# Kernel optimization log

Measured on AMD Instinct MI355X. Metric: run time of the kernel, lower is better.

Reference implementation:

```python
import jax, jax.numpy as jnp
import numpy as np

N, E, G = 100000, 400000, 4096
H, C = 4, 32            # heads, hidden_dim per head
D_OUT = H * C           # 128
NODE_D, EDGE_D = 38, 13
DEC_H, OUT_D = 64, 1
NEG_SLOPE = 0.2
LN_EPS = 1e-5


def setup_inputs() -> dict:
    key = jax.random.key(0)
    ks = jax.random.split(key, 40)
    r = lambda k, s: jax.random.normal(k, s, jnp.float32) * 0.1
    inp = {
        "x": jax.random.normal(ks[0], (N, NODE_D), jnp.float32),
        "edge_index": jax.random.randint(ks[1], (2, E), 0, N),
        "edge_attr": jax.random.uniform(ks[2], (E, EDGE_D), jnp.float32),
        "batch": jnp.sort(jax.random.randint(ks[3], (N,), 0, G)),
        # --- block 1 (in=38) ---
        "Wl1": r(ks[4], (NODE_D, D_OUT)), "bl1": jnp.zeros((D_OUT,), jnp.float32),
        "Wr1": r(ks[5], (NODE_D, D_OUT)), "br1": jnp.zeros((D_OUT,), jnp.float32),
        "We1": r(ks[6], (EDGE_D, D_OUT)),
        "att1": r(ks[7], (H, C)), "ab1": jnp.zeros((D_OUT,), jnp.float32),
        "ln_g1": jnp.ones((D_OUT,), jnp.float32), "ln_b1": jnp.zeros((D_OUT,), jnp.float32),
        "Wres": r(ks[8], (NODE_D, D_OUT)), "bres": jnp.zeros((D_OUT,), jnp.float32),
        # --- block 2 (in=128, residual = identity) ---
        "Wl2": r(ks[9], (D_OUT, D_OUT)), "bl2": jnp.zeros((D_OUT,), jnp.float32),
        "Wr2": r(ks[10], (D_OUT, D_OUT)), "br2": jnp.zeros((D_OUT,), jnp.float32),
        "We2": r(ks[11], (EDGE_D, D_OUT)),
        "att2": r(ks[12], (H, C)), "ab2": jnp.zeros((D_OUT,), jnp.float32),
        "ln_g2": jnp.ones((D_OUT,), jnp.float32), "ln_b2": jnp.zeros((D_OUT,), jnp.float32),
        # --- readout MLP ---
        "Wd1": r(ks[13], (D_OUT, DEC_H)), "bd1": jnp.zeros((DEC_H,), jnp.float32),
        "Wd2": r(ks[14], (DEC_H, OUT_D)), "bd2": jnp.zeros((OUT_D,), jnp.float32),
    }
    return inp


def _segment_softmax(logits, seg, n):
    m = jax.ops.segment_max(logits, seg, num_segments=n)
    ex = jnp.exp(logits - m[seg])
    s = jax.ops.segment_sum(ex, seg, num_segments=n)
    return ex / s[seg]


def _gatv2(x, src, dst, e_feat, Wl, bl, Wr, br, We, att, ab):
    n = x.shape[0]
    xl = (x @ Wl + bl).reshape(n, H, C)   # source transform
    xr = (x @ Wr + br).reshape(n, H, C)   # target transform
    ee = (e_feat @ We).reshape(-1, H, C)  # edge transform
    z = jax.nn.leaky_relu(xl[src] + xr[dst] + ee, NEG_SLOPE)  # [E,H,C]
    logits = jnp.einsum('ehc,hc->eh', z, att)                 # [E,H]
    alpha = _segment_softmax(logits, dst, n)                  # softmax over target nbhd
    out = jax.ops.segment_sum(xl[src] * alpha[..., None], dst, num_segments=n)
    return out.reshape(n, D_OUT) + ab


def _layernorm(h, g, b):
    mu = jnp.mean(h, -1, keepdims=True)
    d = h - mu
    v = jnp.mean(d * d, -1, keepdims=True)
    return d * jax.lax.rsqrt(v + LN_EPS) * g + b


def reference(x, edge_index, edge_attr, batch,
              Wl1, bl1, Wr1, br1, We1, att1, ab1, ln_g1, ln_b1, Wres, bres,
              Wl2, bl2, Wr2, br2, We2, att2, ab2, ln_g2, ln_b2,
              Wd1, bd1, Wd2, bd2):
    src, dst = edge_index[0], edge_index[1]
    n = x.shape[0]
    # add_self_loops(fill_value='mean'): self-loop edge attr = mean of incoming edge attrs
    deg = jax.ops.segment_sum(jnp.ones((src.shape[0],), x.dtype), dst, num_segments=n)
    loop_attr = jax.ops.segment_sum(edge_attr, dst, num_segments=n) / jnp.clip(deg, 1.0)[:, None]
    nodes = jnp.arange(n)
    src_a = jnp.concatenate([src, nodes])
    dst_a = jnp.concatenate([dst, nodes])
    ea = jnp.concatenate([edge_attr, loop_attr], axis=0)

    # block 1
    h = _gatv2(x, src_a, dst_a, ea, Wl1, bl1, Wr1, br1, We1, att1, ab1)
    h = jax.nn.elu(h)
    h = _layernorm(h + (x @ Wres + bres), ln_g1, ln_b1)
    # block 2 (identity residual)
    h2 = _gatv2(h, src_a, dst_a, ea, Wl2, bl2, Wr2, br2, We2, att2, ab2)
    h2 = jax.nn.elu(h2)
    h2 = _layernorm(h2 + h, ln_g2, ln_b2)

    # global mean pool over graphs
    cnt = jax.ops.segment_sum(jnp.ones((n,), x.dtype), batch, num_segments=G)
    g = jax.ops.segment_sum(h2, batch, num_segments=G) / jnp.clip(cnt, 1.0)[:, None]

    return jax.nn.relu(g @ Wd1 + bd1) @ Wd2 + bd2
```

## Files before the change

kernel.cpp:

```cpp
#include <hip/hip_runtime.h>

typedef unsigned short u16;
typedef unsigned int   u32;
typedef __attribute__((ext_vector_type(8))) short short8;
typedef __attribute__((ext_vector_type(4))) float float4v;
typedef __attribute__((ext_vector_type(2))) float float2v;

#define NODE_D   38
#define EDGE_D   13
#define D_OUT    128
#define NEG_SLOPE 0.2f
#define LN_EPS   1e-5f

__device__ __forceinline__ float bf2f(u16 v) { return __uint_as_float(((u32)v) << 16); }
__device__ __forceinline__ u16 f2bf(float f) {
    u32 u = __float_as_uint(f);
    u += 0x7fffu + ((u >> 16) & 1u);
    return (u16)(u >> 16);
}

template <int CTRL>
__device__ __forceinline__ float dpp_radd(float x) {
    int t = __builtin_amdgcn_update_dpp(0, __float_as_int(x), CTRL, 0xf, 0xf, true);
    return x + __int_as_float(t);
}
__device__ __forceinline__ float reduce16(float p) {
    p = dpp_radd<0xB1>(p);
    p = dpp_radd<0x4E>(p);
    p = dpp_radd<0x124>(p);
    p = dpp_radd<0x128>(p);
    return p;
}
__device__ __forceinline__ float reduce64(float v) {
    v = reduce16(v);
    v += __shfl_xor(v, 16, 64);
    v += __shfl_xor(v, 32, 64);
    return v;
}

__global__ void k_pre(const int* __restrict__ dst, int E, int* __restrict__ deg,
                      const int* __restrict__ batch, int N, int G, int* __restrict__ goff,
                      const float* __restrict__ x, u16* __restrict__ xb) {
    int i = blockIdx.x * blockDim.x + threadIdx.x;
    if (i < E) atomicAdd(deg + dst[i], 1);
    if (i < N) {
        int b = batch[i];
        int prev = (i == 0) ? -1 : batch[i - 1];
        for (int g = prev + 1; g <= b; g++) goff[g] = i;
        if (i == N - 1)
            for (int g = b + 1; g <= G; g++) goff[g] = N;
    }
    if (i < N * 32) {
        int n = i >> 5, kk = (i & 31) * 2;
        float f0 = (kk < NODE_D) ? x[(size_t)n * NODE_D + kk] : 0.f;
        float f1 = (kk + 1 < NODE_D) ? x[(size_t)n * NODE_D + kk + 1] : 0.f;
        ((u32*)xb)[(size_t)n * 32 + (i & 31)] = (u32)f2bf(f0) | ((u32)f2bf(f1) << 16);
    }
}

#define SCAN_CHUNK 1024
__global__ void k_scan1(const int* __restrict__ cnt, int N, int addone, int* __restrict__ bsum) {
    __shared__ int sh[256];
    int base = blockIdx.x * SCAN_CHUNK;
    int t = threadIdx.x;
    int s = 0;
#pragma unroll
    for (int i = 0; i < 4; i++) { int idx = base + t * 4 + i; if (idx < N) s += cnt[idx] + addone; }
    sh[t] = s; __syncthreads();
    for (int ofs = 128; ofs > 0; ofs >>= 1) {
        if (t < ofs) sh[t] += sh[t + ofs];
        __syncthreads();
    }
    if (t == 0) bsum[blockIdx.x] = sh[0];
}
__global__ void k_scan2(const int* __restrict__ bsum, int nb, int* __restrict__ boff) {
    __shared__ int sh[256];
    int t = threadIdx.x;
    if (nb <= 256) {
        int v = (t < nb) ? bsum[t] : 0;
        sh[t] = v; __syncthreads();
        for (int ofs = 1; ofs < 256; ofs <<= 1) {
            int x = (t >= ofs) ? sh[t - ofs] : 0;
            __syncthreads();
            sh[t] += x;
            __syncthreads();
        }
        if (t < nb) boff[t] = sh[t] - v;
        if (t == nb - 1) boff[nb] = sh[t];
    } else if (t == 0) {
        int run = 0;
        for (int i = 0; i < nb; i++) { boff[i] = run; run += bsum[i]; }
        boff[nb] = run;
    }
}
__global__ void k_scan3(const int* __restrict__ cnt, int N, int addone,
                        const int* __restrict__ boff, int nb, int* __restrict__ off) {
    __shared__ int wtot[4];
    int base = blockIdx.x * SCAN_CHUNK;
    int t = threadIdx.x;
    int lane = t & 63, w = t >> 6;
    int v[4]; int s = 0;
#pragma unroll
    for (int i = 0; i < 4; i++) { int idx = base + t * 4 + i; v[i] = (idx < N) ? cnt[idx] + addone : 0; s += v[i]; }
    int inc = s;
#pragma unroll
    for (int ofs = 1; ofs < 64; ofs <<= 1) {
        int x = __shfl_up(inc, ofs, 64);
        if (lane >= ofs) inc += x;
    }
    if (lane == 63) wtot[w] = inc;
    __syncthreads();
    int wofs = 0;
    for (int i = 0; i < w; i++) wofs += wtot[i];
    int run = boff[blockIdx.x] + wofs + (inc - s);
#pragma unroll
    for (int i = 0; i < 4; i++) {
        int idx = base + t * 4 + i;
        if (idx < N) off[idx] = run;
        run += v[i];
    }
    if (blockIdx.x == 0 && t == 0) off[N] = boff[nb];
}

__global__ void k_fill(const int* __restrict__ src, const int* __restrict__ dst,
                       const float* __restrict__ eattr, int E,
                       const int* __restrict__ csr_off, int* __restrict__ fill,
                       int* __restrict__ csr_src, u16* __restrict__ A) {
    int e = blockIdx.x * blockDim.x + threadIdx.x;
    if (e >= E) return;
    int d = dst[e];
    int pos = csr_off[d] + atomicAdd(fill + d, 1);
    csr_src[pos] = src[e];
    u16 row[16];
#pragma unroll
    for (int k = 0; k < EDGE_D; k++) row[k] = f2bf(eattr[(size_t)e * EDGE_D + k]);
#pragma unroll
    for (int k = EDGE_D; k < 16; k++) row[k] = 0;
    uint4* rp = (uint4*)(A + (size_t)pos * 16);
    rp[0] = (uint4){(u32)row[0] | ((u32)row[1] << 16), (u32)row[2] | ((u32)row[3] << 16),
                    (u32)row[4] | ((u32)row[5] << 16), (u32)row[6] | ((u32)row[7] << 16)};
    rp[1] = (uint4){(u32)row[8] | ((u32)row[9] << 16), (u32)row[10] | ((u32)row[11] << 16),
                    (u32)row[12] | ((u32)row[13] << 16), (u32)row[14] | ((u32)row[15] << 16)};
}

__global__ void k_self(const int* __restrict__ csr_off, int N,
                       int* __restrict__ csr_src, u16* __restrict__ A) {
    int tid = blockIdx.x * blockDim.x + threadIdx.x;
    if (tid >= N * 16) return;
    int n = tid >> 4, k = tid & 15;
    int b = csr_off[n], e2 = csr_off[n + 1] - 1;
    u16 v = 0;
    if (k < EDGE_D) {
        float s = 0.f;
        for (int j = b; j < e2; j++) s += bf2f(A[(size_t)j * 16 + k]);
        v = f2bf(s / fmaxf((float)(e2 - b), 1.f));
    }
    A[(size_t)e2 * 16 + k] = v;
    if (k == 0) csr_src[e2] = n;
}

template <int KPAD, int CT, int KREAL, bool IN_BF16>
__global__ __launch_bounds__(256) void k_tf_mfma(
    const void* __restrict__ in_v,
    const float* __restrict__ W0, const float* __restrict__ b0,
    const float* __restrict__ W1, const float* __restrict__ b1,
    const float* __restrict__ W2, const float* __restrict__ b2,
    u16* __restrict__ o0, u16* __restrict__ o1, u16* __restrict__ o2,
    int N) {
    constexpr int RS = KPAD + 8;
    __shared__ u16 Bsw[CT * 16 * RS];
    __shared__ float bsh[CT * 16];
    const float* Ws[3] = {W0, W1, W2};
    const float* bs[3] = {b0, b1, b2};
    u16* outs[3] = {o0, o1, o2};
    int t = threadIdx.x;
    for (int i = t; i < CT * 16 * KPAD; i += 256) {
        int c = i / KPAD, k = i - c * KPAD;
        float v = (k < KREAL) ? Ws[c >> 7][(size_t)k * 128 + (c & 127)] : 0.f;
        Bsw[c * RS + k] = f2bf(v);
    }
    for (int i = t; i < CT * 16; i += 256) bsh[i] = bs[i >> 7][i & 127];
    __syncthreads();

    int wid = t >> 6, lane = t & 63;
    int quad = lane >> 4, m = lane & 15;

    for (int g0 = blockIdx.x * 64; g0 < N; g0 += gridDim.x * 64) {
        int na = g0 + wid * 16 + m;
        if (na > N - 1) na = N - 1;
        short8 a[KPAD / 32];
        if (IN_BF16) {
            const u16* in = (const u16*)in_v;
#pragma unroll
            for (int kc = 0; kc < KPAD / 32; kc++)
                a[kc] = *(const short8*)(in + (size_t)na * KPAD + kc * 32 + quad * 8);
        } else {
            const float* in = (const float*)in_v;
#pragma unroll
            for (int kc = 0; kc < KPAD / 32; kc++)
#pragma unroll
                for (int j = 0; j < 8; j++) {
                    int k = kc * 32 + quad * 8 + j;
                    float v = (k < KREAL) ? in[(size_t)na * KREAL + k] : 0.f;
                    a[kc][j] = (short)f2bf(v);
                }
        }
        float4v acc[CT];
#pragma unroll
        for (int ct = 0; ct < CT; ct++) acc[ct] = (float4v){0.f, 0.f, 0.f, 0.f};
#pragma unroll
        for (int ct = 0; ct < CT; ct++) {
#pragma unroll
            for (int kc = 0; kc < KPAD / 32; kc++) {
                short8 b = *(const short8*)(&Bsw[(ct * 16 + m) * RS + kc * 32 + quad * 8]);
                acc[ct] = __builtin_amdgcn_mfma_f32_16x16x32_bf16(a[kc], b, acc[ct], 0, 0, 0);
            }
        }
#pragma unroll
        for (int ct = 0; ct < CT; ct++) {
            int col = ct * 16 + m;
            u16* op = outs[col >> 7];
            int cc = col & 127;
            float bv = bsh[col];
#pragma unroll
            for (int r = 0; r < 4; r++) {
                int node = g0 + wid * 16 + quad * 4 + r;
                if (node < N) op[(size_t)node * 128 + cc] = f2bf(acc[ct][r] + bv);
            }
        }
    }
}

__global__ __launch_bounds__(256) void k_gat(
    const int* __restrict__ csr_off, const int* __restrict__ csr_src,
    const u16* __restrict__ A_csr,
    const u16* __restrict__ xl, const u16* __restrict__ xr,
    const u16* __restrict__ res, const float* __restrict__ We,
    const float* __restrict__ att, const float* __restrict__ ab,
    const float* __restrict__ lng, const float* __restrict__ lnb,
    u16* __restrict__ hout, int N, int npw) {
    int t = threadIdx.x;
    int wid = t >> 6, lane = t & 63;
    int wave = blockIdx.x * 4 + wid;
    int n0 = wave * npw;
    if (n0 >= N) return;
    int n1 = n0 + npw; if (n1 > N) n1 = N;

    float2v we2[EDGE_D];
#pragma unroll
    for (int k = 0; k < EDGE_D; k++)
        we2[k] = (float2v){We[k * D_OUT + 2 * lane], We[k * D_OUT + 2 * lane + 1]};
    float a0 = att[2 * lane], a1 = att[2 * lane + 1];
    float abv0 = ab[2 * lane], abv1 = ab[2 * lane + 1];
    float lg0 = lng[2 * lane], lg1 = lng[2 * lane + 1];
    float lb0 = lnb[2 * lane], lb1 = lnb[2 * lane + 1];

    const u32* xl32 = (const u32*)xl;
    const u32* xr32 = (const u32*)xr;
    int wbeg = csr_off[n0];
    int wend = csr_off[n1];
    int nedge = wend - wbeg;

    auto finish = [&](int n, float ssum, float2v acc2) {
        float inv = 1.f / ssum;
        float o0 = acc2[0] * inv + abv0;
        float o1 = acc2[1] * inv + abv1;
        o0 = (o0 > 0.f) ? o0 : (__expf(o0) - 1.f);
        o1 = (o1 > 0.f) ? o1 : (__expf(o1) - 1.f);
        u32 rw = ((const u32*)res)[(size_t)n * 64 + lane];
        o0 += bf2f((u16)(rw & 0xffff));
        o1 += bf2f((u16)(rw >> 16));
        float sm = reduce64(o0 + o1);
        float mu = sm * (1.f / 128.f);
        float d0 = o0 - mu, d1 = o1 - mu;
        float vv = reduce64(d0 * d0 + d1 * d1);
        float rs = rsqrtf(vv * (1.f / 128.f) + LN_EPS);
        float h0 = d0 * rs * lg0 + lb0;
        float h1 = d1 * rs * lg1 + lb1;
        ((u32*)hout)[(size_t)n * 64 + lane] = (u32)f2bf(h0) | ((u32)f2bf(h1) << 16);
    };

    const float2v z0v = (float2v){0.f, 0.f};

    if (nedge <= 64) {
        int last = nedge - 1;
        int sv = csr_src[wbeg + ((lane < nedge) ? lane : last)];
        int f0 = __builtin_amdgcn_readlane(sv, 0);
        int f1 = __builtin_amdgcn_readlane(sv, (1 <= last) ? 1 : last);
        int f2 = __builtin_amdgcn_readlane(sv, (2 <= last) ? 2 : last);
        int f3 = __builtin_amdgcn_readlane(sv, (3 <= last) ? 3 : last);
        u32 xw0 = xl32[(size_t)f0 * 64 + lane];
        u32 xw1 = xl32[(size_t)f1 * 64 + lane];
        u32 xw2 = xl32[(size_t)f2 * 64 + lane];
        u32 xw3 = xl32[(size_t)f3 * 64 + lane];
        const uint4* ap = (const uint4*)(A_csr + (size_t)wbeg * 16);
        uint4 aq0 = ap[0], aq1 = ap[1];

        int i = wbeg;
        for (int n = n0; n < n1; n++) {
            int end = csr_off[n + 1];
            u32 xrw = xr32[(size_t)n * 64 + lane];
            float2v xr2 = (float2v){bf2f((u16)(xrw & 0xffff)), bf2f((u16)(xrw >> 16))};
            float ssum = 0.f;
            float2v acc2 = (float2v){0.f, 0.f};
            for (; i < end; i++) {
                int j4 = i + 4 - wbeg; if (j4 > last) j4 = last;
                int f4 = __builtin_amdgcn_readlane(sv, j4);
                u32 xwN = xl32[(size_t)f4 * 64 + lane];
                int j1n = i + 1 - wbeg; if (j1n > last) j1n = last;
                const uint4* apn = (const uint4*)(A_csr + (size_t)(wbeg + j1n) * 16);
                uint4 an0 = apn[0], an1 = apn[1];

                u32 dw[8] = {aq0.x, aq0.y, aq0.z, aq0.w, aq1.x, aq1.y, aq1.z, aq1.w};
                float2v eeA = (float2v){0.f, 0.f}, eeB = (float2v){0.f, 0.f};
#pragma unroll
                for (int k = 0; k < EDGE_D; k++) {
                    u32 d = dw[k >> 1];
                    float av = __uint_as_float((k & 1) ? (d & 0xffff0000u) : (d << 16));
                    if ((k >> 1) & 1) eeB += we2[k] * av;
                    else             eeA += we2[k] * av;
                }
                float2v xs = (float2v){bf2f((u16)(xw0 & 0xffff)), bf2f((u16)(xw0 >> 16))};
                float2v z = (xs + xr2) + (eeA + eeB);
                float2v lz = __builtin_elementwise_max(z, z0v) + __builtin_elementwise_min(z, z0v) * NEG_SLOPE;
                float p = lz[0] * a0 + lz[1] * a1;
                p = reduce16(p);
                float wgt = __expf(p);
                ssum += wgt;
                acc2 += xs * wgt;
                xw0 = xw1; xw1 = xw2; xw2 = xw3; xw3 = xwN;
                aq0 = an0; aq1 = an1;
            }
            finish(n, ssum, acc2);
        }
    } else {
        int cl = wend - 1;
        int f = csr_src[wbeg];
        u32 xw = xl32[(size_t)f * 64 + lane];
        const uint4* ap = (const uint4*)(A_csr + (size_t)wbeg * 16);
        uint4 aq0 = ap[0], aq1 = ap[1];
        int i = wbeg;
        for (int n = n0; n < n1; n++) {
            int end = csr_off[n + 1];
            u32 xrw = xr32[(size_t)n * 64 + lane];
            float2v xr2 = (float2v){bf2f((u16)(xrw & 0xffff)), bf2f((u16)(xrw >> 16))};
            float ssum = 0.f;
            float2v acc2 = (float2v){0.f, 0.f};
            for (; i < end; i++) {
                u32 xwc = xw; uint4 q0 = aq0, q1 = aq1;
                int ip = (i + 1 < wend) ? i + 1 : cl;
                f = csr_src[ip];
                xw = xl32[(size_t)f * 64 + lane];
                const uint4* ap2 = (const uint4*)(A_csr + (size_t)ip * 16);
                aq0 = ap2[0]; aq1 = ap2[1];
                u32 dw[8] = {q0.x, q0.y, q0.z, q0.w, q1.x, q1.y, q1.z, q1.w};
                float2v eeA = (float2v){0.f, 0.f}, eeB = (float2v){0.f, 0.f};
#pragma unroll
                for (int k = 0; k < EDGE_D; k++) {
                    u32 d = dw[k >> 1];
                    float av = __uint_as_float((k & 1) ? (d & 0xffff0000u) : (d << 16));
                    if ((k >> 1) & 1) eeB += we2[k] * av;
                    else             eeA += we2[k] * av;
                }
                float2v xs = (float2v){bf2f((u16)(xwc & 0xffff)), bf2f((u16)(xwc >> 16))};
                float2v z = (xs + xr2) + (eeA + eeB);
                float2v lz = __builtin_elementwise_max(z, z0v) + __builtin_elementwise_min(z, z0v) * NEG_SLOPE;
                float p = lz[0] * a0 + lz[1] * a1;
                p = reduce16(p);
                float wgt = __expf(p);
                ssum += wgt;
                acc2 += xs * wgt;
            }
            finish(n, ssum, acc2);
        }
    }
}

__global__ __launch_bounds__(256) void k_pool_read(
    const u16* __restrict__ h2, const int* __restrict__ goff,
    const float* __restrict__ Wd1, const float* __restrict__ bd1,
    const float* __restrict__ Wd2, const float* __restrict__ bd2,
    float* __restrict__ out, int G) {
    __shared__ float acc4[4][128];
    __shared__ float psh[128];
    __shared__ float rsh[2][64];
    int g = blockIdx.x;
    int t = threadIdx.x;
    int lane = t & 63, sw = t >> 6;
    int b = goff[g], e = goff[g + 1];
    const u32* h32 = (const u32*)h2;
    float s0 = 0.f, s1 = 0.f;
    for (int n = b + sw; n < e; n += 4) {
        u32 w = h32[(size_t)n * 64 + lane];
        s0 += bf2f((u16)(w & 0xffff));
        s1 += bf2f((u16)(w >> 16));
    }
    acc4[sw][2 * lane] = s0;
    acc4[sw][2 * lane + 1] = s1;
    __syncthreads();
    if (t < 128) {
        float v = acc4[0][t] + acc4[1][t] + acc4[2][t] + acc4[3][t];
        psh[t] = v / fmaxf((float)(e - b), 1.f);
    }
    __syncthreads();
    if (t < 128) {
        int j = t & 63, hw = t >> 6;
        float acc = (hw == 0) ? bd1[j] : 0.f;
        int k0 = hw * 64;
        for (int k = k0; k < k0 + 64; k++)
            acc += psh[k] * Wd1[k * 64 + j];
        rsh[hw][j] = acc;
    }
    __syncthreads();
    if (t < 64) {
        float a = fmaxf(rsh[0][t] + rsh[1][t], 0.f);
        float v = a * Wd2[t];
#pragma unroll
        for (int mk = 1; mk < 64; mk <<= 1) v += __shfl_xor(v, mk, 64);
        if (t == 0) out[g] = v + bd2[0];
    }
}

extern "C" void kernel_launch(void* const* d_in, const int* in_sizes, int n_in,
                              void* d_out, int out_size, void* d_ws, size_t ws_size,
                              hipStream_t stream) {
    const float* x     = (const float*)d_in[0];
    const int*   eidx  = (const int*)d_in[1];
    const float* eattr = (const float*)d_in[2];
    const int*   batch = (const int*)d_in[3];
    const float* Wl1 = (const float*)d_in[4],  *bl1 = (const float*)d_in[5];
    const float* Wr1 = (const float*)d_in[6],  *br1 = (const float*)d_in[7];
    const float* We1 = (const float*)d_in[8],  *att1 = (const float*)d_in[9],  *ab1 = (const float*)d_in[10];
    const float* lng1 = (const float*)d_in[11], *lnb1 = (const float*)d_in[12];
    const float* Wres = (const float*)d_in[13], *bres = (const float*)d_in[14];
    const float* Wl2 = (const float*)d_in[15], *bl2 = (const float*)d_in[16];
    const float* Wr2 = (const float*)d_in[17], *br2 = (const float*)d_in[18];
    const float* We2 = (const float*)d_in[19], *att2 = (const float*)d_in[20], *ab2 = (const float*)d_in[21];
    const float* lng2 = (const float*)d_in[22], *lnb2 = (const float*)d_in[23];
    const float* Wd1 = (const float*)d_in[24], *bd1 = (const float*)d_in[25];
    const float* Wd2 = (const float*)d_in[26], *bd2 = (const float*)d_in[27];

    int N = in_sizes[0] / NODE_D;
    int E = in_sizes[1] / 2;
    int G = out_size;
    int EN = E + N;
    const int* src = eidx;
    const int* dst = eidx + E;

    char* w = (char*)d_ws;
    auto alloc = [&](size_t bytes) -> char* {
        char* p = w;
        w += (bytes + 255) & ~(size_t)255;
        return p;
    };
    int NB = (N + SCAN_CHUNK - 1) / SCAN_CHUNK;
    int*   csr_off  = (int*)alloc((size_t)(N + 1) * 4);
    int*   csr_src  = (int*)alloc((size_t)EN * 4);
    u16*   A_csr    = (u16*)alloc((size_t)(EN + 64) * 16 * 2);
    u16*   xb       = (u16*)alloc((size_t)N * 64 * 2);
    u16*   xlb      = (u16*)alloc((size_t)N * D_OUT * 2);
    u16*   xrb      = (u16*)alloc((size_t)N * D_OUT * 2);
    u16*   resb     = (u16*)alloc((size_t)N * D_OUT * 2);
    u16*   hb       = (u16*)alloc((size_t)N * D_OUT * 2);
    int*   goff     = (int*)alloc((size_t)(G + 1) * 4);
    size_t szN = ((size_t)N * 4 + 255) & ~(size_t)255;
    char*  zp   = alloc(2 * szN);
    int*   deg  = (int*)zp;
    int*   fill = (int*)(zp + szN);
    int*   bsum = (int*)alloc((size_t)(NB + 1) * 4);
    int*   boff = (int*)alloc((size_t)(NB + 1) * 4);

    hipMemsetAsync(zp, 0, 2 * szN, stream);

    int mx = (E > N * 32) ? E : N * 32;
    k_pre<<<(mx + 255) / 256, 256, 0, stream>>>(dst, E, deg, batch, N, G, goff, x, xb);

    k_scan1<<<NB, 256, 0, stream>>>(deg, N, 1, bsum);
    k_scan2<<<1, 256, 0, stream>>>(bsum, NB, boff);
    k_scan3<<<NB, 256, 0, stream>>>(deg, N, 1, boff, NB, csr_off);
    k_fill<<<(E + 255) / 256, 256, 0, stream>>>(src, dst, eattr, E, csr_off, fill, csr_src, A_csr);
    k_self<<<((size_t)N * 16 + 255) / 256, 256, 0, stream>>>(csr_off, N, csr_src, A_csr);

    int npw = 4;
    int gblocks = (N + npw * 4 - 1) / (npw * 4);

    k_tf_mfma<64, 24, NODE_D, true><<<640, 256, 0, stream>>>(
        xb, Wl1, bl1, Wr1, br1, Wres, bres, xlb, xrb, resb, N);
    k_gat<<<gblocks, 256, 0, stream>>>(csr_off, csr_src, A_csr,
                                       xlb, xrb, resb, We1, att1, ab1, lng1, lnb1, hb, N, npw);

    k_tf_mfma<128, 16, 128, true><<<640, 256, 0, stream>>>(
        hb, Wl2, bl2, Wr2, br2, Wr2, br2, xlb, xrb, xrb, N);
    k_gat<<<gblocks, 256, 0, stream>>>(csr_off, csr_src, A_csr,
                                       xlb, xrb, hb, We2, att2, ab2, lng2, lnb2, resb, N, npw);

    k_pool_read<<<G, 256, 0, stream>>>(resb, goff, Wd1, bd1, Wd2, bd2, (float*)d_out, G);
}
```

Baseline: 583.2 us.

## Fuse mean-pool into second GAT via atomics, vectorize MFMA output stores

```diff
diff --git a/kernel.cpp b/kernel.cpp
--- a/kernel.cpp
+++ b/kernel.cpp
@@ -213,19 +213,23 @@
 #pragma unroll
             for (int kc = 0; kc < KPAD / 32; kc++) {
                 short8 b = *(const short8*)(&Bsw[(ct * 16 + m) * RS + kc * 32 + quad * 8]);
-                acc[ct] = __builtin_amdgcn_mfma_f32_16x16x32_bf16(a[kc], b, acc[ct], 0, 0, 0);
+                acc[ct] = __builtin_amdgcn_mfma_f32_16x16x32_bf16(b, a[kc], acc[ct], 0, 0, 0);
             }
         }
-#pragma unroll
-        for (int ct = 0; ct < CT; ct++) {
-            int col = ct * 16 + m;
-            u16* op = outs[col >> 7];
-            int cc = col & 127;
-            float bv = bsh[col];
-#pragma unroll
-            for (int r = 0; r < 4; r++) {
-                int node = g0 + wid * 16 + quad * 4 + r;
-                if (node < N) op[(size_t)node * 128 + cc] = f2bf(acc[ct][r] + bv);
+        int node = g0 + wid * 16 + m;
+        if (node < N) {
+#pragma unroll
+            for (int ct = 0; ct < CT; ct++) {
+                int colb = ct * 16 + quad * 4;
+                u16* op = outs[colb >> 7];
+                int cc = colb & 127;
+                float4v bq = *(const float4v*)&bsh[colb];
+                ushort4 wv;
+                wv.x = f2bf(acc[ct][0] + bq[0]);
+                wv.y = f2bf(acc[ct][1] + bq[1]);
+                wv.z = f2bf(acc[ct][2] + bq[2]);
+                wv.w = f2bf(acc[ct][3] + bq[3]);
+                *(ushort4*)(op + (size_t)node * 128 + cc) = wv;
             }
         }
     }
@@ -238,7 +242,8 @@
     const u16* __restrict__ res, const float* __restrict__ We,
     const float* __restrict__ att, const float* __restrict__ ab,
     const float* __restrict__ lng, const float* __restrict__ lnb,
-    u16* __restrict__ hout, int N, int npw) {
+    u16* __restrict__ hout, const int* __restrict__ batch, float* __restrict__ gsum,
+    int N, int npw) {
     int t = threadIdx.x;
     int wid = t >> 6, lane = t & 63;
     int wave = blockIdx.x * 4 + wid;
@@ -277,7 +282,13 @@
         float rs = rsqrtf(vv * (1.f / 128.f) + LN_EPS);
         float h0 = d0 * rs * lg0 + lb0;
         float h1 = d1 * rs * lg1 + lb1;
-        ((u32*)hout)[(size_t)n * 64 + lane] = (u32)f2bf(h0) | ((u32)f2bf(h1) << 16);
+        if (gsum) {
+            int g = batch[n];
+            atomicAdd(gsum + (size_t)g * 128 + 2 * lane, h0);
+            atomicAdd(gsum + (size_t)g * 128 + 2 * lane + 1, h1);
+        } else {
+            ((u32*)hout)[(size_t)n * 64 + lane] = (u32)f2bf(h0) | ((u32)f2bf(h1) << 16);
+        }
     };
 
     const float2v z0v = (float2v){0.f, 0.f};
@@ -376,41 +387,25 @@
     }
 }
 
-__global__ __launch_bounds__(256) void k_pool_read(
-    const u16* __restrict__ h2, const int* __restrict__ goff,
+__global__ __launch_bounds__(128) void k_read(
+    const float* __restrict__ gsum, const int* __restrict__ goff,
     const float* __restrict__ Wd1, const float* __restrict__ bd1,
     const float* __restrict__ Wd2, const float* __restrict__ bd2,
     float* __restrict__ out, int G) {
-    __shared__ float acc4[4][128];
     __shared__ float psh[128];
     __shared__ float rsh[2][64];
     int g = blockIdx.x;
     int t = threadIdx.x;
-    int lane = t & 63, sw = t >> 6;
-    int b = goff[g], e = goff[g + 1];
-    const u32* h32 = (const u32*)h2;
-    float s0 = 0.f, s1 = 0.f;
-    for (int n = b + sw; n < e; n += 4) {
-        u32 w = h32[(size_t)n * 64 + lane];
-        s0 += bf2f((u16)(w & 0xffff));
-        s1 += bf2f((u16)(w >> 16));
-    }
-    acc4[sw][2 * lane] = s0;
-    acc4[sw][2 * lane + 1] = s1;
+    int cnt = goff[g + 1] - goff[g];
+    float inv = 1.f / fmaxf((float)cnt, 1.f);
+    psh[t] = gsum[(size_t)g * 128 + t] * inv;
     __syncthreads();
-    if (t < 128) {
-        float v = acc4[0][t] + acc4[1][t] + acc4[2][t] + acc4[3][t];
-        psh[t] = v / fmaxf((float)(e - b), 1.f);
-    }
-    __syncthreads();
-    if (t < 128) {
-        int j = t & 63, hw = t >> 6;
-        float acc = (hw == 0) ? bd1[j] : 0.f;
-        int k0 = hw * 64;
-        for (int k = k0; k < k0 + 64; k++)
-            acc += psh[k] * Wd1[k * 64 + j];
-        rsh[hw][j] = acc;
-    }
+    int j = t & 63, hw = t >> 6;
+    float acc = (hw == 0) ? bd1[j] : 0.f;
+    int k0 = hw * 64;
+    for (int k = k0; k < k0 + 64; k++)
+        acc += psh[k] * Wd1[k * 64 + j];
+    rsh[hw][j] = acc;
     __syncthreads();
     if (t < 64) {
         float a = fmaxf(rsh[0][t] + rsh[1][t], 0.f);
@@ -464,13 +459,15 @@
     u16*   hb       = (u16*)alloc((size_t)N * D_OUT * 2);
     int*   goff     = (int*)alloc((size_t)(G + 1) * 4);
     size_t szN = ((size_t)N * 4 + 255) & ~(size_t)255;
-    char*  zp   = alloc(2 * szN);
+    size_t szG = ((size_t)G * 128 * 4 + 255) & ~(size_t)255;
+    char*  zp   = alloc(2 * szN + szG);
     int*   deg  = (int*)zp;
     int*   fill = (int*)(zp + szN);
+    float* gsum = (float*)(zp + 2 * szN);
     int*   bsum = (int*)alloc((size_t)(NB + 1) * 4);
     int*   boff = (int*)alloc((size_t)(NB + 1) * 4);
 
-    hipMemsetAsync(zp, 0, 2 * szN, stream);
+    hipMemsetAsync(zp, 0, 2 * szN + szG, stream);
 
     int mx = (E > N * 32) ? E : N * 32;
     k_pre<<<(mx + 255) / 256, 256, 0, stream>>>(dst, E, deg, batch, N, G, goff, x, xb);
@@ -484,15 +481,17 @@
     int npw = 4;
     int gblocks = (N + npw * 4 - 1) / (npw * 4);
 
-    k_tf_mfma<64, 24, NODE_D, true><<<640, 256, 0, stream>>>(
+    k_tf_mfma<64, 24, NODE_D, true><<<512, 256, 0, stream>>>(
         xb, Wl1, bl1, Wr1, br1, Wres, bres, xlb, xrb, resb, N);
     k_gat<<<gblocks, 256, 0, stream>>>(csr_off, csr_src, A_csr,
-                                       xlb, xrb, resb, We1, att1, ab1, lng1, lnb1, hb, N, npw);
-
-    k_tf_mfma<128, 16, 128, true><<<640, 256, 0, stream>>>(
+                                       xlb, xrb, resb, We1, att1, ab1, lng1, lnb1,
+                                       hb, nullptr, nullptr, N, npw);
+
+    k_tf_mfma<128, 16, 128, true><<<512, 256, 0, stream>>>(
         hb, Wl2, bl2, Wr2, br2, Wr2, br2, xlb, xrb, xrb, N);
     k_gat<<<gblocks, 256, 0, stream>>>(csr_off, csr_src, A_csr,
-                                       xlb, xrb, hb, We2, att2, ab2, lng2, lnb2, resb, N, npw);
-
-    k_pool_read<<<G, 256, 0, stream>>>(resb, goff, Wd1, bd1, Wd2, bd2, (float*)d_out, G);
-}
+                                       xlb, xrb, hb, We2, att2, ab2, lng2, lnb2,
+                                       (u16*)nullptr, batch, gsum, N, npw);
+
+    k_read<<<G, 128, 0, stream>>>(gsum, goff, Wd1, bd1, Wd2, bd2, (float*)d_out, G);
+}
```

Measured after the change: 563.0 us. 3.5% less time.
